# Performance work log

Hardware: AMD Instinct MI355X
Metric: run time of the kernel (lower is better)

Reference implementation:

```python
import jax, jax.numpy as jnp
import numpy as np

DIM = 512
MAXP = 100
N_SAMPLED = MAXP - 2  # partitions 0 (whole) and 1 (singletons) handled analytically
KMAX = 6              # sampled partitions have 2..6 parts


def _make_part_masks(dim, n_sampled, kmax, seed=0):
    rng = np.random.default_rng(seed)
    masks = np.zeros((n_sampled, kmax, dim), dtype=bool)
    for p in range(n_sampled):
        n_parts = rng.integers(2, kmax + 1)
        assign = rng.integers(0, n_parts, size=dim)
        for k in range(n_parts):
            masks[p, k] = assign == k
    return masks


def setup_inputs() -> dict:
    key = jax.random.key(0)
    ks = jax.random.split(key, 10)
    B, S, D = 8, 4096, DIM
    x = jax.random.normal(ks[0], (B, S, D), dtype=jnp.float32)
    entropy_scales = jnp.ones((D,), dtype=jnp.float32)
    integration_weights = jnp.ones((MAXP,), dtype=jnp.float32)
    W1 = jax.random.normal(ks[1], (32, 1), dtype=jnp.float32) * 0.5
    b1 = jax.random.normal(ks[2], (32,), dtype=jnp.float32) * 0.1
    W2 = jax.random.normal(ks[3], (16, 32), dtype=jnp.float32) * 0.2
    b2 = jax.random.normal(ks[4], (16,), dtype=jnp.float32) * 0.1
    W3 = jax.random.normal(ks[5], (1, 16), dtype=jnp.float32) * 0.3
    b3 = jax.random.normal(ks[6], (1,), dtype=jnp.float32) * 0.1
    part_masks = jnp.asarray(_make_part_masks(D, N_SAMPLED, KMAX))  # [P,K,D] bool
    return {"x": x, "entropy_scales": entropy_scales,
            "integration_weights": integration_weights,
            "W1": W1, "b1": b1, "W2": W2, "b2": b2, "W3": W3, "b3": b3,
            "part_masks": part_masks}


def _phi(x, entropy_scales, integration_weights, W1, b1, W2, b2, W3, b3, part_masks):
    B, S, D = x.shape
    # ---- full-flatten entropy (per batch), H(softmax(x.reshape(B,-1))) ----
    lp = jax.nn.log_softmax(x.reshape(B, -1), axis=-1)
    H_full = -jnp.sum(jnp.exp(lp) * lp, axis=-1)                     # [B]
    h_full_scaled = H_full * entropy_scales.mean()                   # [B]
    h_whole = H_full.mean()                                          # partition idx 0

    # ---- singleton partition (idx 1): softmax over seq per (b,d) ----
    lps = jax.nn.log_softmax(x, axis=1)                              # [B,S,D]
    H_sd = -jnp.sum(jnp.exp(lps) * lps, axis=1)                      # [B,D]
    h_single = H_sd.mean(axis=0).sum()

    # ---- sampled partitions via masks: per part, softmax over (seq x part dims) ----
    xmax_d = x.max(axis=1)                                           # [B,D]
    ex = jnp.exp(x - xmax_d[:, None, :])                             # [B,S,D]
    e_d = ex.sum(axis=1)                                             # [B,D] sum exp(x - xmax_d)
    t_d = (ex * x).sum(axis=1)                                       # [B,D] sum exp(.)*x
    valid = part_masks.any(axis=-1)                                  # [P,K]
    neg = jnp.finfo(x.dtype).min
    gmax = jnp.max(jnp.where(part_masks[None], xmax_d[:, None, None, :], neg), axis=-1)  # [B,P,K]
    gmax = jnp.where(valid[None], gmax, 0.0)
    shift = jnp.exp(xmax_d[:, None, None, :] - gmax[..., None])      # [B,P,K,D] <= 1
    mf = part_masks.astype(x.dtype)
    Z = jnp.einsum('pkd,bd,bpkd->bpk', mf, e_d, shift)               # group partition fn
    T = jnp.einsum('pkd,bd,bpkd->bpk', mf, t_d, shift)
    Zs = jnp.where(valid[None], Z, 1.0)
    H_pk = gmax + jnp.log(Zs) - T / Zs                               # group entropy [B,P,K]
    H_pk = jnp.where(valid[None], H_pk, 0.0)
    h_sampled = H_pk.mean(axis=0).sum(axis=-1)                       # [P] sum of part entropies

    h_parts = jnp.concatenate([jnp.stack([h_whole, h_single]), h_sampled])   # [100]
    weighted = h_parts * jax.nn.sigmoid(integration_weights[: h_parts.shape[0]])
    min_part = weighted.min()

    raw_phi = h_full_scaled.mean() - min_part
    z = jnp.clip(raw_phi / 10.0, 0.0, 1.0)[None]                     # [1]
    h = jax.nn.relu(z @ W1.T + b1)
    h = jax.nn.relu(h @ W2.T + b2)
    conf = jax.nn.sigmoid(h @ W3.T + b3).squeeze(-1)                 # scalar
    return conf


def reference(x, entropy_scales, integration_weights, W1, b1, W2, b2, W3, b3, part_masks):
    return _phi(x, entropy_scales, integration_weights, W1, b1, W2, b2, W3, b3, part_masks)
```

## Files before the change

### kernel.cpp

```cpp
#include <hip/hip_runtime.h>
#include <math.h>

constexpr int Bv = 8;
constexpr int Sv = 4096;
constexpr int Dv = 512;
constexpr int NCv = 64;
constexpr int SCv = Sv / NCv;
constexpr int Pv = 98;
constexpr int Kv = 6;
constexpr int MAXPv = 100;

constexpr size_t OFF_MPART = 0;
constexpr size_t OFF_ZPART = OFF_MPART + (size_t)Bv * NCv * Dv;
constexpr size_t OFF_TPART = OFF_ZPART + (size_t)Bv * NCv * Dv;
constexpr size_t OFF_XMAX  = OFF_TPART + (size_t)Bv * NCv * Dv;
constexpr size_t OFF_ED    = OFF_XMAX + (size_t)Bv * Dv;
constexpr size_t OFF_TD    = OFF_ED   + (size_t)Bv * Dv;
constexpr size_t OFF_HFULL = OFF_TD   + (size_t)Bv * Dv;
constexpr size_t OFF_HSD   = OFF_HFULL + Bv;
constexpr size_t OFF_HBP   = OFF_HSD + Bv;

__device__ __forceinline__ float warpSum(float v) {
    for (int o = 32; o > 0; o >>= 1) v += __shfl_xor(v, o);
    return v;
}
__device__ __forceinline__ float warpMax(float v) {
    for (int o = 32; o > 0; o >>= 1) v = fmaxf(v, __shfl_xor(v, o));
    return v;
}
__device__ __forceinline__ float blockSum512(float v, float* red) {
    float s = warpSum(v);
    int lane = threadIdx.x & 63, w = threadIdx.x >> 6;
    __syncthreads();
    if (lane == 0) red[w] = s;
    __syncthreads();
    return red[0] + red[1] + red[2] + red[3] + red[4] + red[5] + red[6] + red[7];
}
__device__ __forceinline__ float blockMax512(float v, float* red) {
    float s = warpMax(v);
    int lane = threadIdx.x & 63, w = threadIdx.x >> 6;
    __syncthreads();
    if (lane == 0) red[w] = s;
    __syncthreads();
    float m = red[0];
    for (int i = 1; i < 8; i++) m = fmaxf(m, red[i]);
    return m;
}

#define UPD(v, m, z, t)                                        \
    {                                                          \
        float vv = (v);                                        \
        if (vv > m) {                                          \
            float r = __expf(m - vv);                          \
            z = z * r + 1.0f;                                  \
            t = t * r + vv;                                    \
            m = vv;                                            \
        } else {                                               \
            float e_ = __expf(vv - m);                         \
            z += e_;                                           \
            t += e_ * vv;                                      \
        }                                                      \
    }

__device__ __forceinline__ void mergeStats(float& m, float& z, float& t,
                                           float mb, float zb, float tb) {
    float nm = fmaxf(m, mb);
    float ra = __expf(m - nm);
    float rb = __expf(mb - nm);
    z = z * ra + zb * rb;
    t = t * ra + tb * rb;
    m = nm;
}

__device__ __forceinline__ float sigmoidf(float v) { return 1.0f / (1.0f + __expf(-v)); }

__global__ __launch_bounds__(256) void k1_partial(const float* __restrict__ x,
                                                  float* __restrict__ ws) {
    int c = blockIdx.x;
    int b = blockIdx.y;
    int tid = threadIdx.x;
    int dg = tid & 127;
    int sl = tid >> 7;

    const float4* xv = (const float4*)x;
    float m0 = -INFINITY, m1 = -INFINITY, m2 = -INFINITY, m3 = -INFINITY;
    float z0 = 0.f, z1 = 0.f, z2 = 0.f, z3 = 0.f;
    float t0 = 0.f, t1 = 0.f, t2 = 0.f, t3 = 0.f;

    int sbase = c * SCv + sl;
    for (int i = 0; i < SCv / 2; i++) {
        int s = sbase + 2 * i;
        float4 v = xv[((size_t)b * Sv + s) * 128 + dg];
        UPD(v.x, m0, z0, t0);
        UPD(v.y, m1, z1, t1);
        UPD(v.z, m2, z2, t2);
        UPD(v.w, m3, z3, t3);
    }

    __shared__ float smm[512], smz[512], smt[512];
    if (sl == 1) {
        smm[dg * 4 + 0] = m0; smm[dg * 4 + 1] = m1; smm[dg * 4 + 2] = m2; smm[dg * 4 + 3] = m3;
        smz[dg * 4 + 0] = z0; smz[dg * 4 + 1] = z1; smz[dg * 4 + 2] = z2; smz[dg * 4 + 3] = z3;
        smt[dg * 4 + 0] = t0; smt[dg * 4 + 1] = t1; smt[dg * 4 + 2] = t2; smt[dg * 4 + 3] = t3;
    }
    __syncthreads();
    if (sl == 0) {
        mergeStats(m0, z0, t0, smm[dg * 4 + 0], smz[dg * 4 + 0], smt[dg * 4 + 0]);
        mergeStats(m1, z1, t1, smm[dg * 4 + 1], smz[dg * 4 + 1], smt[dg * 4 + 1]);
        mergeStats(m2, z2, t2, smm[dg * 4 + 2], smz[dg * 4 + 2], smt[dg * 4 + 2]);
        mergeStats(m3, z3, t3, smm[dg * 4 + 3], smz[dg * 4 + 3], smt[dg * 4 + 3]);

        size_t o = ((size_t)(b * NCv + c)) * 128 + dg;
        ((float4*)(ws + OFF_MPART))[o] = make_float4(m0, m1, m2, m3);
        ((float4*)(ws + OFF_ZPART))[o] = make_float4(z0, z1, z2, z3);
        ((float4*)(ws + OFF_TPART))[o] = make_float4(t0, t1, t2, t3);
    }
}

__global__ __launch_bounds__(512) void k2_combine(float* __restrict__ ws) {
    int b = blockIdx.x;
    int d = threadIdx.x;
    const float* mp = ws + OFF_MPART;
    const float* zp = ws + OFF_ZPART;
    const float* tp = ws + OFF_TPART;

    float m = -INFINITY, z = 0.f, t = 0.f;
    for (int c = 0; c < NCv; c++) {
        size_t idx = ((size_t)(b * NCv + c)) * Dv + d;
        mergeStats(m, z, t, mp[idx], zp[idx], tp[idx]);
    }

    ws[OFF_XMAX + (size_t)b * Dv + d] = m;
    ws[OFF_ED   + (size_t)b * Dv + d] = z;
    ws[OFF_TD   + (size_t)b * Dv + d] = t;

    float hsd = m + __logf(z) - t / z;

    __shared__ float red[8];
    float sum_h = blockSum512(hsd, red);
    float mb = blockMax512(m, red);
    float sc = __expf(m - mb);
    float zb = blockSum512(z * sc, red);
    float tb = blockSum512(t * sc, red);
    if (d == 0) {
        ws[OFF_HSD + b] = sum_h;
        ws[OFF_HFULL + b] = mb + __logf(zb) - tb / zb;
    }
}

__global__ __launch_bounds__(512) void k3_parts(const void* __restrict__ masks,
                                                float* __restrict__ ws) {
    int p = blockIdx.x;
    int b = blockIdx.y;
    int d = threadIdx.x;
    int lane = d & 63, w = d >> 6;

    __shared__ int f;
    if (d == 0) f = 0;
    __syncthreads();
    const unsigned int* mwords = (const unsigned int*)masks;
    if (mwords[d] > 1u) f = 1;
    __syncthreads();

    int mk = 255;
    if (f) {
        const unsigned char* mbyt = (const unsigned char*)masks;
        for (int k = 0; k < Kv; k++)
            if (mbyt[((size_t)p * Kv + k) * Dv + d]) { mk = k; break; }
    } else {
        const int* mint = (const int*)masks;
        for (int k = 0; k < Kv; k++)
            if (mint[((size_t)p * Kv + k) * Dv + d]) { mk = k; break; }
    }

    float xm = ws[OFF_XMAX + (size_t)b * Dv + d];
    float e  = ws[OFF_ED   + (size_t)b * Dv + d];
    float t  = ws[OFF_TD   + (size_t)b * Dv + d];

    __shared__ float lmax[8 * Kv], lz[8 * Kv], lt[8 * Kv];
    __shared__ float gmax[Kv], hk[Kv];

    for (int k = 0; k < Kv; k++) {
        float cv = (mk == k) ? xm : -INFINITY;
        float wm = warpMax(cv);
        if (lane == 0) lmax[w * Kv + k] = wm;
    }
    __syncthreads();
    if (d < Kv) {
        float g = lmax[d];
        for (int ww = 1; ww < 8; ww++) g = fmaxf(g, lmax[ww * Kv + d]);
        gmax[d] = g;
    }
    __syncthreads();

    int mks = (mk < Kv) ? mk : 0;
    float g = gmax[mks];
    float s = __expf(xm - g);
    float ez = e * s, tz = t * s;
    for (int k = 0; k < Kv; k++) {
        float cz = (mk == k) ? ez : 0.f;
        float ctv = (mk == k) ? tz : 0.f;
        float sz = warpSum(cz);
        float st = warpSum(ctv);
        if (lane == 0) { lz[w * Kv + k] = sz; lt[w * Kv + k] = st; }
    }
    __syncthreads();
    if (d < Kv) {
        float Z = 0.f, T = 0.f;
        for (int ww = 0; ww < 8; ww++) { Z += lz[ww * Kv + d]; T += lt[ww * Kv + d]; }
        float gm = gmax[d];
        hk[d] = (gm > -INFINITY) ? gm + __logf(Z) - T / Z : 0.f;
    }
    __syncthreads();
    if (d == 0)
        ws[OFF_HBP + (size_t)b * Pv + p] = hk[0] + hk[1] + hk[2] + hk[3] + hk[4] + hk[5];
}

__global__ __launch_bounds__(128) void k4_final(
    const float* __restrict__ es, const float* __restrict__ iw,
    const float* __restrict__ W1, const float* __restrict__ b1,
    const float* __restrict__ W2, const float* __restrict__ b2,
    const float* __restrict__ W3, const float* __restrict__ b3,
    const float* __restrict__ ws, float* __restrict__ out) {
    int tid = threadIdx.x;
    __shared__ float wgt[MAXPv];
    __shared__ float meanH_s;
    __shared__ float red[2];

    float v = es[tid] + es[tid + 128] + es[tid + 256] + es[tid + 384];
    float s64 = warpSum(v);
    int lane = tid & 63, w = tid >> 6;
    if (lane == 0) red[w] = s64;
    __syncthreads();
    float es_mean = (red[0] + red[1]) * (1.0f / 512.0f);

    if (tid < Pv) {
        float s = 0.f;
        for (int b = 0; b < Bv; b++) s += ws[OFF_HBP + (size_t)b * Pv + tid];
        wgt[tid + 2] = (s * (1.0f / Bv)) * sigmoidf(iw[tid + 2]);
    } else if (tid == Pv) {
        float s = 0.f;
        for (int b = 0; b < Bv; b++) s += ws[OFF_HFULL + b];
        float mh = s * (1.0f / Bv);
        meanH_s = mh;
        wgt[0] = mh * sigmoidf(iw[0]);
    } else if (tid == Pv + 1) {
        float s = 0.f;
        for (int b = 0; b < Bv; b++) s += ws[OFF_HSD + b];
        wgt[1] = (s * (1.0f / Bv)) * sigmoidf(iw[1]);
    }
    __syncthreads();

    if (tid == 0) {
        float mn = wgt[0];
        for (int i = 1; i < MAXPv; i++) mn = fminf(mn, wgt[i]);
        float raw = es_mean * meanH_s - mn;
        float z = fminf(fmaxf(raw * 0.1f, 0.0f), 1.0f);

        float h1[32];
        for (int j = 0; j < 32; j++) {
            float a = z * W1[j] + b1[j];
            h1[j] = a > 0.f ? a : 0.f;
        }
        float h2[16];
        for (int i = 0; i < 16; i++) {
            float a = b2[i];
            for (int j = 0; j < 32; j++) a += W2[i * 32 + j] * h1[j];
            h2[i] = a > 0.f ? a : 0.f;
        }
        float a = b3[0];
        for (int i = 0; i < 16; i++) a += W3[i] * h2[i];
        out[0] = sigmoidf(a);
    }
}

extern "C" void kernel_launch(void* const* d_in, const int* in_sizes, int n_in,
                              void* d_out, int out_size, void* d_ws, size_t ws_size,
                              hipStream_t stream) {
    const float* x  = (const float*)d_in[0];
    const float* es = (const float*)d_in[1];
    const float* iw = (const float*)d_in[2];
    const float* W1 = (const float*)d_in[3];
    const float* b1 = (const float*)d_in[4];
    const float* W2 = (const float*)d_in[5];
    const float* b2 = (const float*)d_in[6];
    const float* W3 = (const float*)d_in[7];
    const float* b3 = (const float*)d_in[8];
    const void* masks = d_in[9];
    float* ws = (float*)d_ws;
    float* out = (float*)d_out;

    k1_partial<<<dim3(NCv, Bv), dim3(256), 0, stream>>>(x, ws);
    k2_combine<<<dim3(Bv), dim3(512), 0, stream>>>(ws);
    k3_parts<<<dim3(Pv, Bv), dim3(512), 0, stream>>>(masks, ws);
    k4_final<<<dim3(1), dim3(128), 0, stream>>>(es, iw, W1, b1, W2, b2, W3, b3, ws, out);
}
```

Baseline: 155.6 us.

## Fuse combine into partition kernel and widen streaming reduction blocks

The separate combine kernel is merged into the partition kernel. Each of 14x8 blocks now redundantly merges the 64 chunk partials for its batch and then loops over 7 partitions, so one launch and the workspace round trip for the per-(b,d) stats go away. The first kernel moves to 512 threads with four sequence lanes, nontemporal vector loads, unrolling and a two-level shared-memory merge. The trade-offs are redundant combine work in every block, fewer blocks in the partition stage, and serialized partition iterations with extra barriers.

```diff
diff --git a/kernel.cpp b/kernel.cpp
--- a/kernel.cpp
+++ b/kernel.cpp
@@ -9,14 +9,15 @@
 constexpr int Pv = 98;
 constexpr int Kv = 6;
 constexpr int MAXPv = 100;
+constexpr int GPv = 14;
+constexpr int PPGv = 7;
+
+typedef float v4f __attribute__((ext_vector_type(4)));
 
 constexpr size_t OFF_MPART = 0;
 constexpr size_t OFF_ZPART = OFF_MPART + (size_t)Bv * NCv * Dv;
 constexpr size_t OFF_TPART = OFF_ZPART + (size_t)Bv * NCv * Dv;
-constexpr size_t OFF_XMAX  = OFF_TPART + (size_t)Bv * NCv * Dv;
-constexpr size_t OFF_ED    = OFF_XMAX + (size_t)Bv * Dv;
-constexpr size_t OFF_TD    = OFF_ED   + (size_t)Bv * Dv;
-constexpr size_t OFF_HFULL = OFF_TD   + (size_t)Bv * Dv;
+constexpr size_t OFF_HFULL = OFF_TPART + (size_t)Bv * NCv * Dv;
 constexpr size_t OFF_HSD   = OFF_HFULL + Bv;
 constexpr size_t OFF_HBP   = OFF_HSD + Bv;
 
@@ -74,7 +75,7 @@
 
 __device__ __forceinline__ float sigmoidf(float v) { return 1.0f / (1.0f + __expf(-v)); }
 
-__global__ __launch_bounds__(256) void k1_partial(const float* __restrict__ x,
+__global__ __launch_bounds__(512) void k1_partial(const float* __restrict__ x,
                                                   float* __restrict__ ws) {
     int c = blockIdx.x;
     int b = blockIdx.y;
@@ -82,138 +83,156 @@
     int dg = tid & 127;
     int sl = tid >> 7;
 
-    const float4* xv = (const float4*)x;
+    const v4f* xv = (const v4f*)x;
     float m0 = -INFINITY, m1 = -INFINITY, m2 = -INFINITY, m3 = -INFINITY;
     float z0 = 0.f, z1 = 0.f, z2 = 0.f, z3 = 0.f;
     float t0 = 0.f, t1 = 0.f, t2 = 0.f, t3 = 0.f;
 
     int sbase = c * SCv + sl;
-    for (int i = 0; i < SCv / 2; i++) {
-        int s = sbase + 2 * i;
-        float4 v = xv[((size_t)b * Sv + s) * 128 + dg];
+#pragma unroll 4
+    for (int i = 0; i < SCv / 4; i++) {
+        int s = sbase + 4 * i;
+        v4f v = __builtin_nontemporal_load(&xv[((size_t)b * Sv + s) * 128 + dg]);
         UPD(v.x, m0, z0, t0);
         UPD(v.y, m1, z1, t1);
         UPD(v.z, m2, z2, t2);
         UPD(v.w, m3, z3, t3);
     }
 
-    __shared__ float smm[512], smz[512], smt[512];
-    if (sl == 1) {
-        smm[dg * 4 + 0] = m0; smm[dg * 4 + 1] = m1; smm[dg * 4 + 2] = m2; smm[dg * 4 + 3] = m3;
-        smz[dg * 4 + 0] = z0; smz[dg * 4 + 1] = z1; smz[dg * 4 + 2] = z2; smz[dg * 4 + 3] = z3;
-        smt[dg * 4 + 0] = t0; smt[dg * 4 + 1] = t1; smt[dg * 4 + 2] = t2; smt[dg * 4 + 3] = t3;
+    __shared__ float smm[1024], smz[1024], smt[1024];
+    if (sl == 1 || sl == 3) {
+        int base = (sl >> 1) * 512 + dg * 4;
+        smm[base + 0] = m0; smm[base + 1] = m1; smm[base + 2] = m2; smm[base + 3] = m3;
+        smz[base + 0] = z0; smz[base + 1] = z1; smz[base + 2] = z2; smz[base + 3] = z3;
+        smt[base + 0] = t0; smt[base + 1] = t1; smt[base + 2] = t2; smt[base + 3] = t3;
+    }
+    __syncthreads();
+    if (sl == 0 || sl == 2) {
+        int base = (sl >> 1) * 512 + dg * 4;
+        mergeStats(m0, z0, t0, smm[base + 0], smz[base + 0], smt[base + 0]);
+        mergeStats(m1, z1, t1, smm[base + 1], smz[base + 1], smt[base + 1]);
+        mergeStats(m2, z2, t2, smm[base + 2], smz[base + 2], smt[base + 2]);
+        mergeStats(m3, z3, t3, smm[base + 3], smz[base + 3], smt[base + 3]);
+    }
+    __syncthreads();
+    if (sl == 2) {
+        int base = dg * 4;
+        smm[base + 0] = m0; smm[base + 1] = m1; smm[base + 2] = m2; smm[base + 3] = m3;
+        smz[base + 0] = z0; smz[base + 1] = z1; smz[base + 2] = z2; smz[base + 3] = z3;
+        smt[base + 0] = t0; smt[base + 1] = t1; smt[base + 2] = t2; smt[base + 3] = t3;
     }
     __syncthreads();
     if (sl == 0) {
-        mergeStats(m0, z0, t0, smm[dg * 4 + 0], smz[dg * 4 + 0], smt[dg * 4 + 0]);
-        mergeStats(m1, z1, t1, smm[dg * 4 + 1], smz[dg * 4 + 1], smt[dg * 4 + 1]);
-        mergeStats(m2, z2, t2, smm[dg * 4 + 2], smz[dg * 4 + 2], smt[dg * 4 + 2]);
-        mergeStats(m3, z3, t3, smm[dg * 4 + 3], smz[dg * 4 + 3], smt[dg * 4 + 3]);
+        int base = dg * 4;
+        mergeStats(m0, z0, t0, smm[base + 0], smz[base + 0], smt[base + 0]);
+        mergeStats(m1, z1, t1, smm[base + 1], smz[base + 1], smt[base + 1]);
+        mergeStats(m2, z2, t2, smm[base + 2], smz[base + 2], smt[base + 2]);
+        mergeStats(m3, z3, t3, smm[base + 3], smz[base + 3], smt[base + 3]);
 
         size_t o = ((size_t)(b * NCv + c)) * 128 + dg;
-        ((float4*)(ws + OFF_MPART))[o] = make_float4(m0, m1, m2, m3);
-        ((float4*)(ws + OFF_ZPART))[o] = make_float4(z0, z1, z2, z3);
-        ((float4*)(ws + OFF_TPART))[o] = make_float4(t0, t1, t2, t3);
-    }
-}
-
-__global__ __launch_bounds__(512) void k2_combine(float* __restrict__ ws) {
-    int b = blockIdx.x;
+        ((v4f*)(ws + OFF_MPART))[o] = (v4f){m0, m1, m2, m3};
+        ((v4f*)(ws + OFF_ZPART))[o] = (v4f){z0, z1, z2, z3};
+        ((v4f*)(ws + OFF_TPART))[o] = (v4f){t0, t1, t2, t3};
+    }
+}
+
+__global__ __launch_bounds__(512) void k23_parts(const void* __restrict__ masks,
+                                                 float* __restrict__ ws) {
+    int g = blockIdx.x;
+    int b = blockIdx.y;
     int d = threadIdx.x;
+    int lane = d & 63, w = d >> 6;
+
     const float* mp = ws + OFF_MPART;
     const float* zp = ws + OFF_ZPART;
     const float* tp = ws + OFF_TPART;
 
-    float m = -INFINITY, z = 0.f, t = 0.f;
-    for (int c = 0; c < NCv; c++) {
-        size_t idx = ((size_t)(b * NCv + c)) * Dv + d;
-        mergeStats(m, z, t, mp[idx], zp[idx], tp[idx]);
-    }
-
-    ws[OFF_XMAX + (size_t)b * Dv + d] = m;
-    ws[OFF_ED   + (size_t)b * Dv + d] = z;
-    ws[OFF_TD   + (size_t)b * Dv + d] = t;
-
-    float hsd = m + __logf(z) - t / z;
+    float ma = -INFINITY, za = 0.f, ta = 0.f;
+    float mb2 = -INFINITY, zb2 = 0.f, tb2 = 0.f;
+    for (int c = 0; c < NCv / 2; c++) {
+        size_t ia = ((size_t)(b * NCv + c)) * Dv + d;
+        size_t ib = ((size_t)(b * NCv + c + NCv / 2)) * Dv + d;
+        mergeStats(ma, za, ta, mp[ia], zp[ia], tp[ia]);
+        mergeStats(mb2, zb2, tb2, mp[ib], zp[ib], tp[ib]);
+    }
+    mergeStats(ma, za, ta, mb2, zb2, tb2);
+    float xm = ma, e = za, t = ta;
 
     __shared__ float red[8];
-    float sum_h = blockSum512(hsd, red);
-    float mb = blockMax512(m, red);
-    float sc = __expf(m - mb);
-    float zb = blockSum512(z * sc, red);
-    float tb = blockSum512(t * sc, red);
-    if (d == 0) {
-        ws[OFF_HSD + b] = sum_h;
-        ws[OFF_HFULL + b] = mb + __logf(zb) - tb / zb;
-    }
-}
-
-__global__ __launch_bounds__(512) void k3_parts(const void* __restrict__ masks,
-                                                float* __restrict__ ws) {
-    int p = blockIdx.x;
-    int b = blockIdx.y;
-    int d = threadIdx.x;
-    int lane = d & 63, w = d >> 6;
+    if (g == 0) {
+        float hsd = xm + __logf(e) - t / e;
+        float sum_h = blockSum512(hsd, red);
+        float mbk = blockMax512(xm, red);
+        float sc = __expf(xm - mbk);
+        float zb = blockSum512(e * sc, red);
+        float tb = blockSum512(t * sc, red);
+        if (d == 0) {
+            ws[OFF_HSD + b] = sum_h;
+            ws[OFF_HFULL + b] = mbk + __logf(zb) - tb / zb;
+        }
+    }
 
     __shared__ int f;
     if (d == 0) f = 0;
     __syncthreads();
-    const unsigned int* mwords = (const unsigned int*)masks;
-    if (mwords[d] > 1u) f = 1;
-    __syncthreads();
-
-    int mk = 255;
-    if (f) {
-        const unsigned char* mbyt = (const unsigned char*)masks;
-        for (int k = 0; k < Kv; k++)
-            if (mbyt[((size_t)p * Kv + k) * Dv + d]) { mk = k; break; }
-    } else {
-        const int* mint = (const int*)masks;
-        for (int k = 0; k < Kv; k++)
-            if (mint[((size_t)p * Kv + k) * Dv + d]) { mk = k; break; }
-    }
-
-    float xm = ws[OFF_XMAX + (size_t)b * Dv + d];
-    float e  = ws[OFF_ED   + (size_t)b * Dv + d];
-    float t  = ws[OFF_TD   + (size_t)b * Dv + d];
+    if (((const unsigned int*)masks)[d] > 1u) f = 1;
+    __syncthreads();
+    int is_u8 = f;
 
     __shared__ float lmax[8 * Kv], lz[8 * Kv], lt[8 * Kv];
     __shared__ float gmax[Kv], hk[Kv];
 
-    for (int k = 0; k < Kv; k++) {
-        float cv = (mk == k) ? xm : -INFINITY;
-        float wm = warpMax(cv);
-        if (lane == 0) lmax[w * Kv + k] = wm;
-    }
-    __syncthreads();
-    if (d < Kv) {
-        float g = lmax[d];
-        for (int ww = 1; ww < 8; ww++) g = fmaxf(g, lmax[ww * Kv + d]);
-        gmax[d] = g;
-    }
-    __syncthreads();
-
-    int mks = (mk < Kv) ? mk : 0;
-    float g = gmax[mks];
-    float s = __expf(xm - g);
-    float ez = e * s, tz = t * s;
-    for (int k = 0; k < Kv; k++) {
-        float cz = (mk == k) ? ez : 0.f;
-        float ctv = (mk == k) ? tz : 0.f;
-        float sz = warpSum(cz);
-        float st = warpSum(ctv);
-        if (lane == 0) { lz[w * Kv + k] = sz; lt[w * Kv + k] = st; }
-    }
-    __syncthreads();
-    if (d < Kv) {
-        float Z = 0.f, T = 0.f;
-        for (int ww = 0; ww < 8; ww++) { Z += lz[ww * Kv + d]; T += lt[ww * Kv + d]; }
-        float gm = gmax[d];
-        hk[d] = (gm > -INFINITY) ? gm + __logf(Z) - T / Z : 0.f;
-    }
-    __syncthreads();
-    if (d == 0)
-        ws[OFF_HBP + (size_t)b * Pv + p] = hk[0] + hk[1] + hk[2] + hk[3] + hk[4] + hk[5];
+    for (int i = 0; i < PPGv; i++) {
+        int p = g * PPGv + i;
+
+        int mk = 255;
+        if (is_u8) {
+            const unsigned char* mbyt = (const unsigned char*)masks;
+            for (int k = 0; k < Kv; k++)
+                if (mbyt[((size_t)p * Kv + k) * Dv + d]) { mk = k; break; }
+        } else {
+            const int* mint = (const int*)masks;
+            for (int k = 0; k < Kv; k++)
+                if (mint[((size_t)p * Kv + k) * Dv + d]) { mk = k; break; }
+        }
+
+        for (int k = 0; k < Kv; k++) {
+            float cv = (mk == k) ? xm : -INFINITY;
+            float wm = warpMax(cv);
+            if (lane == 0) lmax[w * Kv + k] = wm;
+        }
+        __syncthreads();
+        if (d < Kv) {
+            float gm = lmax[d];
+            for (int ww = 1; ww < 8; ww++) gm = fmaxf(gm, lmax[ww * Kv + d]);
+            gmax[d] = gm;
+        }
+        __syncthreads();
+
+        int mks = (mk < Kv) ? mk : 0;
+        float gm = gmax[mks];
+        float s = __expf(xm - gm);
+        float ez = e * s, tz = t * s;
+        for (int k = 0; k < Kv; k++) {
+            float cz = (mk == k) ? ez : 0.f;
+            float ctv = (mk == k) ? tz : 0.f;
+            float sz = warpSum(cz);
+            float st = warpSum(ctv);
+            if (lane == 0) { lz[w * Kv + k] = sz; lt[w * Kv + k] = st; }
+        }
+        __syncthreads();
+        if (d < Kv) {
+            float Z = 0.f, T = 0.f;
+            for (int ww = 0; ww < 8; ww++) { Z += lz[ww * Kv + d]; T += lt[ww * Kv + d]; }
+            float gmv = gmax[d];
+            hk[d] = (gmv > -INFINITY) ? gmv + __logf(Z) - T / Z : 0.f;
+        }
+        __syncthreads();
+        if (d == 0)
+            ws[OFF_HBP + (size_t)b * Pv + p] =
+                hk[0] + hk[1] + hk[2] + hk[3] + hk[4] + hk[5];
+        __syncthreads();
+    }
 }
 
 __global__ __launch_bounds__(128) void k4_final(
@@ -290,8 +309,7 @@
     float* ws = (float*)d_ws;
     float* out = (float*)d_out;
 
-    k1_partial<<<dim3(NCv, Bv), dim3(256), 0, stream>>>(x, ws);
-    k2_combine<<<dim3(Bv), dim3(512), 0, stream>>>(ws);
-    k3_parts<<<dim3(Pv, Bv), dim3(512), 0, stream>>>(masks, ws);
+    k1_partial<<<dim3(NCv, Bv), dim3(512), 0, stream>>>(x, ws);
+    k23_parts<<<dim3(GPv, Bv), dim3(512), 0, stream>>>(masks, ws);
     k4_final<<<dim3(1), dim3(128), 0, stream>>>(es, iw, W1, b1, W2, b2, W3, b3, ws, out);
 }
```

New measurement: 166.8 us. 1.07x slower.
